# Performance work log

Hardware: AMD Instinct MI355X
Metric: run time of the kernel (lower is better)

Reference implementation:

```python
import jax, jax.numpy as jnp
import numpy as np

# ---- static hyperparams (from comp_encoding.__init__ / DMPNNEncoderLayer) ----
B = 512            # number of molecules in the batch (wrapper's python loop)
A = 128            # padded atoms per molecule == max_mol_len
E = 256            # padded directed bonds per molecule
K = 6              # max incoming bonds gathered per bond/atom
ATOM_FDIM = 133
BOND_FDIM = 14
H = 128            # d_hidden = max_mol_len
DEPTH = 3
G = 2048           # global feature dim (Morgan fingerprint)


def _mol_lens():
    ml = np.array(jax.random.randint(jax.random.fold_in(jax.random.key(0), 5), (B,), 16, H + 1))
    ml[0] = H  # ensure comp_dim == max(mol_lens) == H so per-row padding is a no-op
    return ml


def setup_inputs() -> dict:
    key = jax.random.key(0)
    ks = jax.random.split(key, 10)
    atom_feature = jax.random.normal(ks[0], (B, A, ATOM_FDIM), jnp.float32)
    f_ini_atoms_bond = jax.random.normal(ks[1], (B, E, ATOM_FDIM + BOND_FDIM), jnp.float32)
    atom_to_incoming_bond = jax.random.randint(ks[2], (B, A, K), 0, E)
    mapping = jax.random.randint(ks[3], (B, E, K), 0, E)
    global_f = jax.random.normal(ks[4], (B, G), jnp.float32)
    mol_lens = _mol_lens()  # static numpy ints (constants, drive output shapes)
    W_i = jax.random.normal(ks[6], (H, ATOM_FDIM + BOND_FDIM), jnp.float32) / np.float32(np.sqrt(ATOM_FDIM + BOND_FDIM))
    W_h = jax.random.normal(ks[7], (H, H), jnp.float32) / np.float32(np.sqrt(H))
    W_o = jax.random.normal(ks[8], (H, ATOM_FDIM + H), jnp.float32) / np.float32(np.sqrt(ATOM_FDIM + H))
    b_o = jax.random.normal(ks[9], (H,), jnp.float32) * 0.01
    return dict(atom_feature=atom_feature, f_ini_atoms_bond=f_ini_atoms_bond,
                atom_to_incoming_bond=atom_to_incoming_bond, mapping=mapping,
                global_f=global_f, mol_lens=mol_lens,
                W_i=W_i, W_h=W_h, W_o=W_o, b_o=b_o)


def _gather_sum(msg, idx):
    # msg: [B, E, H]; idx: [B, N, K] -> sum over K incoming messages: [B, N, H]
    b, n, k = idx.shape
    g = jnp.take_along_axis(msg, idx.reshape(b, n * k)[..., None], axis=1)
    return g.reshape(b, n, k, -1).sum(axis=2)


def reference(atom_feature, f_ini_atoms_bond, atom_to_incoming_bond, mapping,
              global_f, mol_lens, W_i, W_h, W_o, b_o):
    # DMPNN: W_i on initial directed-bond features
    inp = jnp.einsum('bef,hf->beh', f_ini_atoms_bond, W_i)   # [B, E, H]
    msg = jax.nn.relu(inp)
    for _ in range(DEPTH - 1):
        agg = _gather_sum(msg, mapping)                      # [B, E, H]
        msg = jax.nn.relu(inp + jnp.einsum('beh,gh->beg', agg, W_h))
    m2a = _gather_sum(msg, atom_to_incoming_bond)            # [B, A, H]
    cat = jnp.concatenate([atom_feature, m2a], axis=-1)      # [B, A, 133+H]
    atoms_h = jax.nn.relu(jnp.einsum('bad,hd->bah', cat, W_o) + b_o)  # [B, A, H]

    # wrapper: take first mol_len atom encodings per molecule, stack, build mask
    ml = np.asarray(mol_lens)
    valid = np.arange(A)[None, :] < ml[:, None]              # [B, A] static
    b_idx, a_idx = np.nonzero(valid)
    comp = atoms_h[b_idx, a_idx]                             # [sum(mol_lens), H]
    c_mask = jnp.asarray(valid.astype(np.float32))           # [B, comp_dim]
    return comp, c_mask
```

## Files before the change

kernel.cpp:

```cpp
#include <hip/hip_runtime.h>
#include <hip/hip_bf16.h>

typedef unsigned int   uint;
typedef unsigned short ushort;
typedef short bf16x8 __attribute__((ext_vector_type(8)));
typedef float f32x4  __attribute__((ext_vector_type(4)));

constexpr int Bm   = 512;
constexpr int Aa   = 128;
constexpr int Ee   = 256;
constexpr int Kk   = 6;
constexpr int AFD  = 133;
constexpr int FD   = 147;
constexpr int Hh   = 128;
constexpr int CATD = 261;
constexpr int KF   = 152;
constexpr int KA   = 144;
constexpr int KWO  = 320;
constexpr int KWIW = 192;
constexpr int LDA  = 72;

__device__ __forceinline__ ushort f2b(float f) {
    uint u = __float_as_uint(f);
    u += 0x7FFFu + ((u >> 16) & 1u);
    return (ushort)(u >> 16);
}
__device__ __forceinline__ uint f2b2(float x, float y) {
    return (uint)f2b(x) | ((uint)f2b(y) << 16);
}
__device__ __forceinline__ float2 b2f2(uint p) {
    float2 r;
    r.x = __uint_as_float(p << 16);
    r.y = __uint_as_float(p & 0xFFFF0000u);
    return r;
}
__device__ __forceinline__ float b2f(ushort u) {
    return __uint_as_float(((uint)u) << 16);
}
__device__ __forceinline__ uint relu2u(uint u) {
    uint neg  = u & 0x80008000u;
    uint mask = (neg >> 15) * 0xFFFFu;
    return u & ~mask;
}

__device__ __forceinline__ void mfma_chunk(const ushort* At, const ushort* Bt,
                                           int wr, int wc, int l15, int quad,
                                           f32x4 acc[4][4]) {
#pragma unroll
    for (int ks = 0; ks < 2; ++ks) {
        const int ko = ks * 32 + quad * 8;
        bf16x8 af[4], bf[4];
#pragma unroll
        for (int i = 0; i < 4; ++i)
            af[i] = *(const bf16x8*)&At[(wr * 64 + i * 16 + l15) * LDA + ko];
#pragma unroll
        for (int j = 0; j < 4; ++j)
            bf[j] = *(const bf16x8*)&Bt[(wc * 64 + j * 16 + l15) * LDA + ko];
#pragma unroll
        for (int i = 0; i < 4; ++i)
#pragma unroll
            for (int j = 0; j < 4; ++j)
                acc[i][j] = __builtin_amdgcn_mfma_f32_16x16x32_bf16(
                    af[i], bf[j], acc[i][j], 0, 0, 0);
    }
}

__global__ __launch_bounds__(256) void k_prep_f(const float* __restrict__ fini,
                                                ushort* __restrict__ fini_b) {
    const int lane = threadIdx.x & 63;
    const int wg   = blockIdx.x * 4 + (threadIdx.x >> 6);
    for (int row = wg; row < Bm * Ee; row += 4096) {
        const float* src = fini + (size_t)row * FD;
        ushort* dst = fini_b + (size_t)row * KF;
        float v0 = src[lane];
        float v1 = src[64 + lane];
        float v2 = (lane < FD - 128) ? src[128 + lane] : 0.f;
        dst[lane]      = f2b(v0);
        dst[64 + lane] = f2b(v1);
        if (lane < KF - 128) dst[128 + lane] = f2b(v2);
    }
}

__global__ __launch_bounds__(256) void k_prep_a(const float* __restrict__ atomf,
                                                ushort* __restrict__ atomf_b) {
    const int lane = threadIdx.x & 63;
    const int wg   = blockIdx.x * 4 + (threadIdx.x >> 6);
    for (int row = wg; row < Bm * Aa; row += 2048) {
        const float* src = atomf + (size_t)row * AFD;
        ushort* dst = atomf_b + (size_t)row * KA;
        float v0 = src[lane];
        float v1 = (lane < AFD - 64) ? src[64 + lane] : 0.f;
        float v2 = (lane < AFD - 128) ? src[128 + lane] : 0.f;
        dst[lane]      = f2b(v0);
        dst[64 + lane] = f2b(v1);
        if (lane < KA - 128) dst[128 + lane] = f2b(v2);
    }
}

__global__ __launch_bounds__(256) void k_prep_w(const float* __restrict__ Wi,
                                                const float* __restrict__ Wh,
                                                const float* __restrict__ Wo,
                                                ushort* __restrict__ Wi_b,
                                                ushort* __restrict__ Wh_b,
                                                ushort* __restrict__ Wo_b) {
    const int h = blockIdx.x, t = threadIdx.x;
    for (int c = t; c < KWIW; c += 256)
        Wi_b[h * KWIW + c] = f2b(c < FD ? Wi[h * FD + c] : 0.f);
    for (int c = t; c < Hh; c += 256)
        Wh_b[h * Hh + c] = f2b(Wh[h * Hh + c]);
    for (int c = t; c < KWO; c += 256) {
        float v = 0.f;
        if (c < AFD)       v = Wo[h * CATD + c];
        else if (c >= 192) v = Wo[h * CATD + AFD + (c - 192)];
        Wo_b[h * KWO + c] = f2b(v);
    }
}

__global__ __launch_bounds__(256, 4) void k_wi(const ushort* __restrict__ fini_b,
                                               const ushort* __restrict__ Wi_b,
                                               ushort* __restrict__ inp_b) {
    __shared__ ushort At[128 * LDA];
    __shared__ ushort Bt[128 * LDA];
    const int tid = threadIdx.x;
    const int row0 = blockIdx.x * 128;
    const int wave = tid >> 6, lane = tid & 63;
    const int wr = wave & 1, wc = wave >> 1;
    const int l15 = lane & 15, quad = lane >> 4;
    f32x4 acc[4][4] = {};

    for (int c = 0; c < 3; ++c) {
        for (int idx = tid; idx < 128 * 8; idx += 256) {
            int r = idx >> 3, g = idx & 7;
            uint4 v = {0, 0, 0, 0};
            if (c < 2 || g < 3)
                v = *(const uint4*)&fini_b[(size_t)(row0 + r) * KF + c * 64 + g * 8];
            *(uint4*)&At[r * LDA + g * 8] = v;
        }
        for (int idx = tid; idx < 128 * 8; idx += 256) {
            int h = idx >> 3, g = idx & 7;
            *(uint4*)&Bt[h * LDA + g * 8] =
                *(const uint4*)&Wi_b[h * KWIW + c * 64 + g * 8];
        }
        __syncthreads();
        mfma_chunk(At, Bt, wr, wc, l15, quad, acc);
        __syncthreads();
    }
#pragma unroll
    for (int i = 0; i < 4; ++i)
#pragma unroll
        for (int reg = 0; reg < 4; ++reg) {
            int row = row0 + wr * 64 + i * 16 + quad * 4 + reg;
#pragma unroll
            for (int j = 0; j < 4; ++j) {
                int col = wc * 64 + j * 16 + l15;
                inp_b[(size_t)row * Hh + col] = f2b(acc[i][j][reg]);
            }
        }
}

__global__ __launch_bounds__(256, 4) void k_hop(const ushort* __restrict__ hIn,
                                                const int* __restrict__ mapping,
                                                const ushort* __restrict__ Wh_b,
                                                const ushort* __restrict__ inp_b,
                                                ushort* __restrict__ hOut) {
    __shared__ ushort At[128 * LDA];
    __shared__ ushort Bt[128 * LDA];
    __shared__ int    map_s[128 * Kk];
    const int tid = threadIdx.x;
    const int row0 = blockIdx.x * 128;
    const int bBase = row0 & ~(Ee - 1);
    const int wave = tid >> 6, lane = tid & 63;
    const int wr = wave & 1, wc = wave >> 1;
    const int l15 = lane & 15, quad = lane >> 4;
    f32x4 acc[4][4] = {};

    for (int i = tid; i < 128 * Kk; i += 256) map_s[i] = mapping[row0 * Kk + i];
    __syncthreads();

    for (int c = 0; c < 2; ++c) {
        for (int t = tid; t < 128 * 8; t += 256) {
            int r = t >> 3, g = t & 7;
            const int* mp = &map_s[r * Kk];
            float2 s0 = {0.f, 0.f}, s1 = {0.f, 0.f}, s2 = {0.f, 0.f}, s3 = {0.f, 0.f};
#pragma unroll
            for (int k = 0; k < Kk; ++k) {
                uint4 m8 = *(const uint4*)
                    &hIn[(size_t)(bBase + mp[k]) * Hh + c * 64 + g * 8];
                float2 a = b2f2(relu2u(m8.x)); s0.x += a.x; s0.y += a.y;
                float2 b = b2f2(relu2u(m8.y)); s1.x += b.x; s1.y += b.y;
                float2 d = b2f2(relu2u(m8.z)); s2.x += d.x; s2.y += d.y;
                float2 e = b2f2(relu2u(m8.w)); s3.x += e.x; s3.y += e.y;
            }
            uint4 o;
            o.x = f2b2(s0.x, s0.y); o.y = f2b2(s1.x, s1.y);
            o.z = f2b2(s2.x, s2.y); o.w = f2b2(s3.x, s3.y);
            *(uint4*)&At[r * LDA + g * 8] = o;
        }
        for (int idx = tid; idx < 128 * 8; idx += 256) {
            int h = idx >> 3, g = idx & 7;
            *(uint4*)&Bt[h * LDA + g * 8] =
                *(const uint4*)&Wh_b[h * Hh + c * 64 + g * 8];
        }
        __syncthreads();
        mfma_chunk(At, Bt, wr, wc, l15, quad, acc);
        __syncthreads();
    }
#pragma unroll
    for (int i = 0; i < 4; ++i)
#pragma unroll
        for (int reg = 0; reg < 4; ++reg) {
            int row = row0 + wr * 64 + i * 16 + quad * 4 + reg;
#pragma unroll
            for (int j = 0; j < 4; ++j) {
                int col = wc * 64 + j * 16 + l15;
                float v = b2f(inp_b[(size_t)row * Hh + col]) + acc[i][j][reg];
                hOut[(size_t)row * Hh + col] = f2b(v);
            }
        }
}

__global__ __launch_bounds__(256, 4) void k_read(const ushort* __restrict__ h2,
                                                 const int* __restrict__ a2ib,
                                                 const ushort* __restrict__ atomf_b,
                                                 const ushort* __restrict__ Wo_b,
                                                 const float* __restrict__ bo,
                                                 const int* __restrict__ mol_lens,
                                                 const int* __restrict__ pfx,
                                                 float* __restrict__ out) {
    __shared__ ushort At[128 * LDA];
    __shared__ ushort Bt[128 * LDA];
    __shared__ int    a2_s[128 * Kk];
    const int tid = threadIdx.x;
    const int b = blockIdx.x;
    const int row0 = b * Aa;
    const int bBase = b * Ee;
    const int wave = tid >> 6, lane = tid & 63;
    const int wr = wave & 1, wc = wave >> 1;
    const int l15 = lane & 15, quad = lane >> 4;
    f32x4 acc[4][4] = {};

    for (int i = tid; i < 128 * Kk; i += 256) a2_s[i] = a2ib[row0 * Kk + i];
    __syncthreads();

    for (int c = 0; c < 5; ++c) {
        if (c < 3) {
            for (int idx = tid; idx < 128 * 8; idx += 256) {
                int r = idx >> 3, g = idx & 7;
                uint4 v = {0, 0, 0, 0};
                if (c < 2 || g < 2)
                    v = *(const uint4*)&atomf_b[(size_t)(row0 + r) * KA + c * 64 + g * 8];
                *(uint4*)&At[r * LDA + g * 8] = v;
            }
        } else {
            const int hb = (c - 3) * 64;
            for (int t = tid; t < 128 * 8; t += 256) {
                int r = t >> 3, g = t & 7;
                const int* mp = &a2_s[r * Kk];
                float2 s0 = {0.f, 0.f}, s1 = {0.f, 0.f}, s2 = {0.f, 0.f}, s3 = {0.f, 0.f};
#pragma unroll
                for (int k = 0; k < Kk; ++k) {
                    uint4 m8 = *(const uint4*)
                        &h2[(size_t)(bBase + mp[k]) * Hh + hb + g * 8];
                    float2 a  = b2f2(relu2u(m8.x)); s0.x += a.x;  s0.y += a.y;
                    float2 bb = b2f2(relu2u(m8.y)); s1.x += bb.x; s1.y += bb.y;
                    float2 d  = b2f2(relu2u(m8.z)); s2.x += d.x;  s2.y += d.y;
                    float2 e  = b2f2(relu2u(m8.w)); s3.x += e.x;  s3.y += e.y;
                }
                uint4 o;
                o.x = f2b2(s0.x, s0.y); o.y = f2b2(s1.x, s1.y);
                o.z = f2b2(s2.x, s2.y); o.w = f2b2(s3.x, s3.y);
                *(uint4*)&At[r * LDA + g * 8] = o;
            }
        }
        for (int idx = tid; idx < 128 * 8; idx += 256) {
            int h = idx >> 3, g = idx & 7;
            *(uint4*)&Bt[h * LDA + g * 8] =
                *(const uint4*)&Wo_b[h * KWO + c * 64 + g * 8];
        }
        __syncthreads();
        mfma_chunk(At, Bt, wr, wc, l15, quad, acc);
        __syncthreads();
    }

    const int len  = mol_lens[b];
    const int base = pfx[b];
#pragma unroll
    for (int i = 0; i < 4; ++i)
#pragma unroll
        for (int reg = 0; reg < 4; ++reg) {
            int a = wr * 64 + i * 16 + quad * 4 + reg;
            if (a < len) {
#pragma unroll
                for (int j = 0; j < 4; ++j) {
                    int col = wc * 64 + j * 16 + l15;
                    float v = acc[i][j][reg] + bo[col];
                    out[(size_t)(base + a) * Hh + col] = v > 0.f ? v : 0.f;
                }
            }
        }
}

__global__ __launch_bounds__(512) void k_scan(const int* __restrict__ ml,
                                              int* __restrict__ pfx) {
    __shared__ int s[512];
    int t = threadIdx.x;
    s[t] = ml[t];
    __syncthreads();
    for (int off = 1; off < 512; off <<= 1) {
        int v = (t >= off) ? s[t - off] : 0;
        __syncthreads();
        s[t] += v;
        __syncthreads();
    }
    pfx[t + 1] = s[t];
    if (t == 0) pfx[0] = 0;
}

__global__ __launch_bounds__(128) void k_cmask(const int* __restrict__ ml,
                                               float* __restrict__ cmask) {
    int b = blockIdx.x, t = threadIdx.x;
    cmask[b * Aa + t] = (t < ml[b]) ? 1.0f : 0.0f;
}

extern "C" void kernel_launch(void* const* d_in, const int* in_sizes, int n_in,
                              void* d_out, int out_size, void* d_ws, size_t ws_size,
                              hipStream_t stream) {
    const float* atom_feature = (const float*)d_in[0];
    const float* f_ini        = (const float*)d_in[1];
    const int*   a2ib         = (const int*)d_in[2];
    const int*   mapping      = (const int*)d_in[3];
    const int*   mol_lens     = (const int*)d_in[5];
    const float* Wi           = (const float*)d_in[6];
    const float* Wh           = (const float*)d_in[7];
    const float* Wo           = (const float*)d_in[8];
    const float* bo           = (const float*)d_in[9];
    float* out = (float*)d_out;

    constexpr size_t NMSG  = (size_t)Bm * Ee * Hh;
    constexpr size_t NFINI = (size_t)Bm * Ee * KF;
    constexpr size_t NATM  = (size_t)Bm * Aa * KA;
    ushort* fini_b  = (ushort*)d_ws;
    ushort* h2      = fini_b;
    ushort* inp_b   = fini_b + NFINI;
    ushort* h1      = inp_b + NMSG;
    ushort* atomf_b = h1 + NMSG;
    ushort* Wi_b    = atomf_b + NATM;
    ushort* Wh_b    = Wi_b + 128 * KWIW;
    ushort* Wo_b    = Wh_b + 128 * Hh;
    int*    pfx     = (int*)(Wo_b + 128 * KWO);

    float* cmask = out + ((size_t)out_size - (size_t)Bm * Aa);

    k_prep_w<<<128, 256, 0, stream>>>(Wi, Wh, Wo, Wi_b, Wh_b, Wo_b);
    k_prep_f<<<1024, 256, 0, stream>>>(f_ini, fini_b);
    k_prep_a<<<512, 256, 0, stream>>>(atom_feature, atomf_b);
    k_scan <<<1, 512, 0, stream>>>(mol_lens, pfx);
    k_cmask<<<Bm, 128, 0, stream>>>(mol_lens, cmask);
    k_wi   <<<(Bm * Ee) / 128, 256, 0, stream>>>(fini_b, Wi_b, inp_b);
    k_hop  <<<(Bm * Ee) / 128, 256, 0, stream>>>(inp_b, mapping, Wh_b, inp_b, h1);
    k_hop  <<<(Bm * Ee) / 128, 256, 0, stream>>>(h1, mapping, Wh_b, inp_b, h2);
    k_read <<<Bm, 256, 0, stream>>>(h2, a2ib, atomf_b, Wo_b, bo,
                                    mol_lens, pfx, out);
}
```

Measured before the change: 304.2 us.

## Fuse whole DMPNN pipeline into one per-molecule kernel with LDS-resident messages

Replaces the separate prep, W_i, two hop, readout and cmask kernels with a single kernel that runs one block per molecule. All bond messages stay in shared memory across the hops, and the fp32 inputs are converted to bf16 on the fly. This removes the global-memory round trips for intermediate bf16 tensors and several kernel launches. In exchange it uses about 140KB of LDS per block, which limits occupancy, and weight fragments are now read from global memory in every block.

Measured after the change: 287.5 us. -5.5%, faster.

```diff
diff --git a/kernel.cpp b/kernel.cpp
--- a/kernel.cpp
+++ b/kernel.cpp
@@ -1,5 +1,4 @@
 #include <hip/hip_runtime.h>
-#include <hip/hip_bf16.h>
 
 typedef unsigned int   uint;
 typedef unsigned short ushort;
@@ -14,11 +13,10 @@
 constexpr int FD   = 147;
 constexpr int Hh   = 128;
 constexpr int CATD = 261;
-constexpr int KF   = 152;
-constexpr int KA   = 144;
+constexpr int KWI  = 192;
 constexpr int KWO  = 320;
-constexpr int KWIW = 192;
-constexpr int LDA  = 72;
+constexpr int MST  = 136;
+constexpr int SST  = 72;
 
 __device__ __forceinline__ ushort f2b(float f) {
     uint u = __float_as_uint(f);
@@ -34,67 +32,23 @@
     r.y = __uint_as_float(p & 0xFFFF0000u);
     return r;
 }
-__device__ __forceinline__ float b2f(ushort u) {
-    return __uint_as_float(((uint)u) << 16);
-}
-__device__ __forceinline__ uint relu2u(uint u) {
-    uint neg  = u & 0x80008000u;
-    uint mask = (neg >> 15) * 0xFFFFu;
-    return u & ~mask;
-}
-
-__device__ __forceinline__ void mfma_chunk(const ushort* At, const ushort* Bt,
-                                           int wr, int wc, int l15, int quad,
-                                           f32x4 acc[4][4]) {
-#pragma unroll
-    for (int ks = 0; ks < 2; ++ks) {
-        const int ko = ks * 32 + quad * 8;
-        bf16x8 af[4], bf[4];
-#pragma unroll
-        for (int i = 0; i < 4; ++i)
-            af[i] = *(const bf16x8*)&At[(wr * 64 + i * 16 + l15) * LDA + ko];
-#pragma unroll
-        for (int j = 0; j < 4; ++j)
-            bf[j] = *(const bf16x8*)&Bt[(wc * 64 + j * 16 + l15) * LDA + ko];
-#pragma unroll
-        for (int i = 0; i < 4; ++i)
-#pragma unroll
-            for (int j = 0; j < 4; ++j)
-                acc[i][j] = __builtin_amdgcn_mfma_f32_16x16x32_bf16(
-                    af[i], bf[j], acc[i][j], 0, 0, 0);
-    }
-}
-
-__global__ __launch_bounds__(256) void k_prep_f(const float* __restrict__ fini,
-                                                ushort* __restrict__ fini_b) {
-    const int lane = threadIdx.x & 63;
-    const int wg   = blockIdx.x * 4 + (threadIdx.x >> 6);
-    for (int row = wg; row < Bm * Ee; row += 4096) {
-        const float* src = fini + (size_t)row * FD;
-        ushort* dst = fini_b + (size_t)row * KF;
-        float v0 = src[lane];
-        float v1 = src[64 + lane];
-        float v2 = (lane < FD - 128) ? src[128 + lane] : 0.f;
-        dst[lane]      = f2b(v0);
-        dst[64 + lane] = f2b(v1);
-        if (lane < KF - 128) dst[128 + lane] = f2b(v2);
-    }
-}
-
-__global__ __launch_bounds__(256) void k_prep_a(const float* __restrict__ atomf,
-                                                ushort* __restrict__ atomf_b) {
-    const int lane = threadIdx.x & 63;
-    const int wg   = blockIdx.x * 4 + (threadIdx.x >> 6);
-    for (int row = wg; row < Bm * Aa; row += 2048) {
-        const float* src = atomf + (size_t)row * AFD;
-        ushort* dst = atomf_b + (size_t)row * KA;
-        float v0 = src[lane];
-        float v1 = (lane < AFD - 64) ? src[64 + lane] : 0.f;
-        float v2 = (lane < AFD - 128) ? src[128 + lane] : 0.f;
-        dst[lane]      = f2b(v0);
-        dst[64 + lane] = f2b(v1);
-        if (lane < KA - 128) dst[128 + lane] = f2b(v2);
-    }
+
+__device__ __forceinline__ bf16x8 gsum6(const ushort* src, const int* mr, int ko) {
+    float2 s0 = {0.f, 0.f}, s1 = {0.f, 0.f}, s2 = {0.f, 0.f}, s3 = {0.f, 0.f};
+#pragma unroll
+    for (int k = 0; k < Kk; ++k) {
+        uint4 m = *(const uint4*)&src[mr[k] + ko];
+        float2 a = b2f2(m.x); s0.x += a.x; s0.y += a.y;
+        float2 b = b2f2(m.y); s1.x += b.x; s1.y += b.y;
+        float2 d = b2f2(m.z); s2.x += d.x; s2.y += d.y;
+        float2 e = b2f2(m.w); s3.x += e.x; s3.y += e.y;
+    }
+    uint4 o;
+    o.x = f2b2(s0.x, s0.y); o.y = f2b2(s1.x, s1.y);
+    o.z = f2b2(s2.x, s2.y); o.w = f2b2(s3.x, s3.y);
+    bf16x8 r;
+    __builtin_memcpy(&r, &o, 16);
+    return r;
 }
 
 __global__ __launch_bounds__(256) void k_prep_w(const float* __restrict__ Wi,
@@ -104,8 +58,8 @@
                                                 ushort* __restrict__ Wh_b,
                                                 ushort* __restrict__ Wo_b) {
     const int h = blockIdx.x, t = threadIdx.x;
-    for (int c = t; c < KWIW; c += 256)
-        Wi_b[h * KWIW + c] = f2b(c < FD ? Wi[h * FD + c] : 0.f);
+    for (int c = t; c < KWI; c += 256)
+        Wi_b[h * KWI + c] = f2b(c < FD ? Wi[h * FD + c] : 0.f);
     for (int c = t; c < Hh; c += 256)
         Wh_b[h * Hh + c] = f2b(Wh[h * Hh + c]);
     for (int c = t; c < KWO; c += 256) {
@@ -114,190 +68,6 @@
         else if (c >= 192) v = Wo[h * CATD + AFD + (c - 192)];
         Wo_b[h * KWO + c] = f2b(v);
     }
-}
-
-__global__ __launch_bounds__(256, 4) void k_wi(const ushort* __restrict__ fini_b,
-                                               const ushort* __restrict__ Wi_b,
-                                               ushort* __restrict__ inp_b) {
-    __shared__ ushort At[128 * LDA];
-    __shared__ ushort Bt[128 * LDA];
-    const int tid = threadIdx.x;
-    const int row0 = blockIdx.x * 128;
-    const int wave = tid >> 6, lane = tid & 63;
-    const int wr = wave & 1, wc = wave >> 1;
-    const int l15 = lane & 15, quad = lane >> 4;
-    f32x4 acc[4][4] = {};
-
-    for (int c = 0; c < 3; ++c) {
-        for (int idx = tid; idx < 128 * 8; idx += 256) {
-            int r = idx >> 3, g = idx & 7;
-            uint4 v = {0, 0, 0, 0};
-            if (c < 2 || g < 3)
-                v = *(const uint4*)&fini_b[(size_t)(row0 + r) * KF + c * 64 + g * 8];
-            *(uint4*)&At[r * LDA + g * 8] = v;
-        }
-        for (int idx = tid; idx < 128 * 8; idx += 256) {
-            int h = idx >> 3, g = idx & 7;
-            *(uint4*)&Bt[h * LDA + g * 8] =
-                *(const uint4*)&Wi_b[h * KWIW + c * 64 + g * 8];
-        }
-        __syncthreads();
-        mfma_chunk(At, Bt, wr, wc, l15, quad, acc);
-        __syncthreads();
-    }
-#pragma unroll
-    for (int i = 0; i < 4; ++i)
-#pragma unroll
-        for (int reg = 0; reg < 4; ++reg) {
-            int row = row0 + wr * 64 + i * 16 + quad * 4 + reg;
-#pragma unroll
-            for (int j = 0; j < 4; ++j) {
-                int col = wc * 64 + j * 16 + l15;
-                inp_b[(size_t)row * Hh + col] = f2b(acc[i][j][reg]);
-            }
-        }
-}
-
-__global__ __launch_bounds__(256, 4) void k_hop(const ushort* __restrict__ hIn,
-                                                const int* __restrict__ mapping,
-                                                const ushort* __restrict__ Wh_b,
-                                                const ushort* __restrict__ inp_b,
-                                                ushort* __restrict__ hOut) {
-    __shared__ ushort At[128 * LDA];
-    __shared__ ushort Bt[128 * LDA];
-    __shared__ int    map_s[128 * Kk];
-    const int tid = threadIdx.x;
-    const int row0 = blockIdx.x * 128;
-    const int bBase = row0 & ~(Ee - 1);
-    const int wave = tid >> 6, lane = tid & 63;
-    const int wr = wave & 1, wc = wave >> 1;
-    const int l15 = lane & 15, quad = lane >> 4;
-    f32x4 acc[4][4] = {};
-
-    for (int i = tid; i < 128 * Kk; i += 256) map_s[i] = mapping[row0 * Kk + i];
-    __syncthreads();
-
-    for (int c = 0; c < 2; ++c) {
-        for (int t = tid; t < 128 * 8; t += 256) {
-            int r = t >> 3, g = t & 7;
-            const int* mp = &map_s[r * Kk];
-            float2 s0 = {0.f, 0.f}, s1 = {0.f, 0.f}, s2 = {0.f, 0.f}, s3 = {0.f, 0.f};
-#pragma unroll
-            for (int k = 0; k < Kk; ++k) {
-                uint4 m8 = *(const uint4*)
-                    &hIn[(size_t)(bBase + mp[k]) * Hh + c * 64 + g * 8];
-                float2 a = b2f2(relu2u(m8.x)); s0.x += a.x; s0.y += a.y;
-                float2 b = b2f2(relu2u(m8.y)); s1.x += b.x; s1.y += b.y;
-                float2 d = b2f2(relu2u(m8.z)); s2.x += d.x; s2.y += d.y;
-                float2 e = b2f2(relu2u(m8.w)); s3.x += e.x; s3.y += e.y;
-            }
-            uint4 o;
-            o.x = f2b2(s0.x, s0.y); o.y = f2b2(s1.x, s1.y);
-            o.z = f2b2(s2.x, s2.y); o.w = f2b2(s3.x, s3.y);
-            *(uint4*)&At[r * LDA + g * 8] = o;
-        }
-        for (int idx = tid; idx < 128 * 8; idx += 256) {
-            int h = idx >> 3, g = idx & 7;
-            *(uint4*)&Bt[h * LDA + g * 8] =
-                *(const uint4*)&Wh_b[h * Hh + c * 64 + g * 8];
-        }
-        __syncthreads();
-        mfma_chunk(At, Bt, wr, wc, l15, quad, acc);
-        __syncthreads();
-    }
-#pragma unroll
-    for (int i = 0; i < 4; ++i)
-#pragma unroll
-        for (int reg = 0; reg < 4; ++reg) {
-            int row = row0 + wr * 64 + i * 16 + quad * 4 + reg;
-#pragma unroll
-            for (int j = 0; j < 4; ++j) {
-                int col = wc * 64 + j * 16 + l15;
-                float v = b2f(inp_b[(size_t)row * Hh + col]) + acc[i][j][reg];
-                hOut[(size_t)row * Hh + col] = f2b(v);
-            }
-        }
-}
-
-__global__ __launch_bounds__(256, 4) void k_read(const ushort* __restrict__ h2,
-                                                 const int* __restrict__ a2ib,
-                                                 const ushort* __restrict__ atomf_b,
-                                                 const ushort* __restrict__ Wo_b,
-                                                 const float* __restrict__ bo,
-                                                 const int* __restrict__ mol_lens,
-                                                 const int* __restrict__ pfx,
-                                                 float* __restrict__ out) {
-    __shared__ ushort At[128 * LDA];
-    __shared__ ushort Bt[128 * LDA];
-    __shared__ int    a2_s[128 * Kk];
-    const int tid = threadIdx.x;
-    const int b = blockIdx.x;
-    const int row0 = b * Aa;
-    const int bBase = b * Ee;
-    const int wave = tid >> 6, lane = tid & 63;
-    const int wr = wave & 1, wc = wave >> 1;
-    const int l15 = lane & 15, quad = lane >> 4;
-    f32x4 acc[4][4] = {};
-
-    for (int i = tid; i < 128 * Kk; i += 256) a2_s[i] = a2ib[row0 * Kk + i];
-    __syncthreads();
-
-    for (int c = 0; c < 5; ++c) {
-        if (c < 3) {
-            for (int idx = tid; idx < 128 * 8; idx += 256) {
-                int r = idx >> 3, g = idx & 7;
-                uint4 v = {0, 0, 0, 0};
-                if (c < 2 || g < 2)
-                    v = *(const uint4*)&atomf_b[(size_t)(row0 + r) * KA + c * 64 + g * 8];
-                *(uint4*)&At[r * LDA + g * 8] = v;
-            }
-        } else {
-            const int hb = (c - 3) * 64;
-            for (int t = tid; t < 128 * 8; t += 256) {
-                int r = t >> 3, g = t & 7;
-                const int* mp = &a2_s[r * Kk];
-                float2 s0 = {0.f, 0.f}, s1 = {0.f, 0.f}, s2 = {0.f, 0.f}, s3 = {0.f, 0.f};
-#pragma unroll
-                for (int k = 0; k < Kk; ++k) {
-                    uint4 m8 = *(const uint4*)
-                        &h2[(size_t)(bBase + mp[k]) * Hh + hb + g * 8];
-                    float2 a  = b2f2(relu2u(m8.x)); s0.x += a.x;  s0.y += a.y;
-                    float2 bb = b2f2(relu2u(m8.y)); s1.x += bb.x; s1.y += bb.y;
-                    float2 d  = b2f2(relu2u(m8.z)); s2.x += d.x;  s2.y += d.y;
-                    float2 e  = b2f2(relu2u(m8.w)); s3.x += e.x;  s3.y += e.y;
-                }
-                uint4 o;
-                o.x = f2b2(s0.x, s0.y); o.y = f2b2(s1.x, s1.y);
-                o.z = f2b2(s2.x, s2.y); o.w = f2b2(s3.x, s3.y);
-                *(uint4*)&At[r * LDA + g * 8] = o;
-            }
-        }
-        for (int idx = tid; idx < 128 * 8; idx += 256) {
-            int h = idx >> 3, g = idx & 7;
-            *(uint4*)&Bt[h * LDA + g * 8] =
-                *(const uint4*)&Wo_b[h * KWO + c * 64 + g * 8];
-        }
-        __syncthreads();
-        mfma_chunk(At, Bt, wr, wc, l15, quad, acc);
-        __syncthreads();
-    }
-
-    const int len  = mol_lens[b];
-    const int base = pfx[b];
-#pragma unroll
-    for (int i = 0; i < 4; ++i)
-#pragma unroll
-        for (int reg = 0; reg < 4; ++reg) {
-            int a = wr * 64 + i * 16 + quad * 4 + reg;
-            if (a < len) {
-#pragma unroll
-                for (int j = 0; j < 4; ++j) {
-                    int col = wc * 64 + j * 16 + l15;
-                    float v = acc[i][j][reg] + bo[col];
-                    out[(size_t)(base + a) * Hh + col] = v > 0.f ? v : 0.f;
-                }
-            }
-        }
 }
 
 __global__ __launch_bounds__(512) void k_scan(const int* __restrict__ ml,
@@ -316,10 +86,217 @@
     if (t == 0) pfx[0] = 0;
 }
 
-__global__ __launch_bounds__(128) void k_cmask(const int* __restrict__ ml,
-                                               float* __restrict__ cmask) {
-    int b = blockIdx.x, t = threadIdx.x;
-    cmask[b * Aa + t] = (t < ml[b]) ? 1.0f : 0.0f;
+__global__ __launch_bounds__(512, 2) void k_fused(
+        const float* __restrict__ atomf,
+        const float* __restrict__ fini,
+        const int*   __restrict__ a2ib,
+        const int*   __restrict__ mapping,
+        const ushort* __restrict__ Wi_b,
+        const ushort* __restrict__ Wh_b,
+        const ushort* __restrict__ Wo_b,
+        const float* __restrict__ bo,
+        const int*   __restrict__ mol_lens,
+        const int*   __restrict__ pfx,
+        float* __restrict__ out,
+        float* __restrict__ cmask) {
+    __shared__ ushort msg0[Ee * MST];
+    __shared__ ushort msg1[Ee * MST];
+    __shared__ int    map_s[Ee * Kk];
+    __shared__ int    a2_s[Aa * Kk];
+
+    const int b    = blockIdx.x;
+    const int tid  = threadIdx.x;
+    const int wave = tid >> 6;
+    const int lane = tid & 63;
+    const int l15  = lane & 15, quad = lane >> 4;
+
+    for (int i = tid; i < Ee * Kk; i += 512) map_s[i] = mapping[b * Ee * Kk + i];
+    for (int i = tid; i < Aa * Kk; i += 512) a2_s[i]  = a2ib[b * Aa * Kk + i];
+    const int len = mol_lens[b];
+    if (tid < Aa) cmask[b * Aa + tid] = (tid < len) ? 1.0f : 0.0f;
+
+    f32x4 acc[2][8];
+#pragma unroll
+    for (int i = 0; i < 2; ++i)
+#pragma unroll
+        for (int j = 0; j < 8; ++j) acc[i][j] = (f32x4){0.f, 0.f, 0.f, 0.f};
+
+    const float* fsrc = fini + (size_t)b * Ee * FD;
+    for (int c = 0; c < 3; ++c) {
+        for (int idx = tid; idx < Ee * 16; idx += 512) {
+            int r = idx >> 4, gg = idx & 15;
+            int c0 = c * 64 + gg * 4;
+            const float* sp = fsrc + (size_t)r * FD + c0;
+            float v0 = (c0 + 0 < FD) ? sp[0] : 0.f;
+            float v1 = (c0 + 1 < FD) ? sp[1] : 0.f;
+            float v2 = (c0 + 2 < FD) ? sp[2] : 0.f;
+            float v3 = (c0 + 3 < FD) ? sp[3] : 0.f;
+            uint2 p;
+            p.x = f2b2(v0, v1);
+            p.y = f2b2(v2, v3);
+            *(uint2*)&msg1[r * SST + gg * 4] = p;
+        }
+        __syncthreads();
+#pragma unroll
+        for (int ks = 0; ks < 2; ++ks) {
+            const int ko = ks * 32 + quad * 8;
+            bf16x8 bf[8], af[2];
+#pragma unroll
+            for (int j = 0; j < 8; ++j)
+                bf[j] = *(const bf16x8*)&Wi_b[(j * 16 + l15) * KWI + c * 64 + ko];
+#pragma unroll
+            for (int i = 0; i < 2; ++i)
+                af[i] = *(const bf16x8*)&msg1[(wave * 32 + i * 16 + l15) * SST + ko];
+#pragma unroll
+            for (int i = 0; i < 2; ++i)
+#pragma unroll
+                for (int j = 0; j < 8; ++j)
+                    acc[i][j] = __builtin_amdgcn_mfma_f32_16x16x32_bf16(
+                        af[i], bf[j], acc[i][j], 0, 0, 0);
+        }
+        __syncthreads();
+    }
+
+    uint2 inp_pk[2][8];
+#pragma unroll
+    for (int i = 0; i < 2; ++i)
+#pragma unroll
+        for (int j = 0; j < 8; ++j) {
+            f32x4 a4 = acc[i][j];
+            uint2 p;
+            p.x = f2b2(a4[0], a4[1]);
+            p.y = f2b2(a4[2], a4[3]);
+            inp_pk[i][j] = p;
+            int col = j * 16 + l15;
+#pragma unroll
+            for (int reg = 0; reg < 4; ++reg) {
+                int row = wave * 32 + i * 16 + quad * 4 + reg;
+                float v = a4[reg] > 0.f ? a4[reg] : 0.f;
+                msg0[row * MST + col] = f2b(v);
+            }
+        }
+    __syncthreads();
+
+#pragma unroll
+    for (int h = 0; h < 2; ++h) {
+        const ushort* src = h ? msg1 : msg0;
+        ushort*       dst = h ? msg0 : msg1;
+        int mr[2][Kk];
+#pragma unroll
+        for (int i = 0; i < 2; ++i) {
+            int row = wave * 32 + i * 16 + l15;
+#pragma unroll
+            for (int k = 0; k < Kk; ++k) mr[i][k] = map_s[row * Kk + k] * MST;
+        }
+#pragma unroll
+        for (int i = 0; i < 2; ++i)
+#pragma unroll
+            for (int j = 0; j < 8; ++j) acc[i][j] = (f32x4){0.f, 0.f, 0.f, 0.f};
+#pragma unroll
+        for (int ks = 0; ks < 4; ++ks) {
+            const int ko = ks * 32 + quad * 8;
+            bf16x8 bf[8], af[2];
+#pragma unroll
+            for (int j = 0; j < 8; ++j)
+                bf[j] = *(const bf16x8*)&Wh_b[(j * 16 + l15) * Hh + ko];
+#pragma unroll
+            for (int i = 0; i < 2; ++i) af[i] = gsum6(src, mr[i], ko);
+#pragma unroll
+            for (int i = 0; i < 2; ++i)
+#pragma unroll
+                for (int j = 0; j < 8; ++j)
+                    acc[i][j] = __builtin_amdgcn_mfma_f32_16x16x32_bf16(
+                        af[i], bf[j], acc[i][j], 0, 0, 0);
+        }
+#pragma unroll
+        for (int i = 0; i < 2; ++i)
+#pragma unroll
+            for (int j = 0; j < 8; ++j) {
+                float2 lo = b2f2(inp_pk[i][j].x);
+                float2 hi = b2f2(inp_pk[i][j].y);
+                float v[4];
+                v[0] = lo.x + acc[i][j][0];
+                v[1] = lo.y + acc[i][j][1];
+                v[2] = hi.x + acc[i][j][2];
+                v[3] = hi.y + acc[i][j][3];
+                int col = j * 16 + l15;
+#pragma unroll
+                for (int reg = 0; reg < 4; ++reg) {
+                    int row = wave * 32 + i * 16 + quad * 4 + reg;
+                    float r = v[reg] > 0.f ? v[reg] : 0.f;
+                    dst[row * MST + col] = f2b(r);
+                }
+            }
+        __syncthreads();
+    }
+
+    f32x4 ro[8];
+#pragma unroll
+    for (int j = 0; j < 8; ++j) ro[j] = (f32x4){0.f, 0.f, 0.f, 0.f};
+
+    const float* asrc = atomf + (size_t)b * Aa * AFD;
+    for (int c = 0; c < 3; ++c) {
+        for (int idx = tid; idx < Aa * 16; idx += 512) {
+            int r = idx >> 4, gg = idx & 15;
+            int c0 = c * 64 + gg * 4;
+            const float* sp = asrc + (size_t)r * AFD + c0;
+            float v0 = (c0 + 0 < AFD) ? sp[0] : 0.f;
+            float v1 = (c0 + 1 < AFD) ? sp[1] : 0.f;
+            float v2 = (c0 + 2 < AFD) ? sp[2] : 0.f;
+            float v3 = (c0 + 3 < AFD) ? sp[3] : 0.f;
+            uint2 p;
+            p.x = f2b2(v0, v1);
+            p.y = f2b2(v2, v3);
+            *(uint2*)&msg1[r * SST + gg * 4] = p;
+        }
+        __syncthreads();
+#pragma unroll
+        for (int ks = 0; ks < 2; ++ks) {
+            const int ko = ks * 32 + quad * 8;
+            bf16x8 a0 = *(const bf16x8*)&msg1[(wave * 16 + l15) * SST + ko];
+            bf16x8 bf[8];
+#pragma unroll
+            for (int j = 0; j < 8; ++j)
+                bf[j] = *(const bf16x8*)&Wo_b[(j * 16 + l15) * KWO + c * 64 + ko];
+#pragma unroll
+            for (int j = 0; j < 8; ++j)
+                ro[j] = __builtin_amdgcn_mfma_f32_16x16x32_bf16(a0, bf[j], ro[j], 0, 0, 0);
+        }
+        __syncthreads();
+    }
+    {
+        int ar[Kk];
+        int row = wave * 16 + l15;
+#pragma unroll
+        for (int k = 0; k < Kk; ++k) ar[k] = a2_s[row * Kk + k] * MST;
+#pragma unroll
+        for (int ks = 0; ks < 4; ++ks) {
+            const int ko = ks * 32 + quad * 8;
+            bf16x8 a0 = gsum6(msg0, ar, ko);
+            bf16x8 bf[8];
+#pragma unroll
+            for (int j = 0; j < 8; ++j)
+                bf[j] = *(const bf16x8*)&Wo_b[(j * 16 + l15) * KWO + 192 + ko];
+#pragma unroll
+            for (int j = 0; j < 8; ++j)
+                ro[j] = __builtin_amdgcn_mfma_f32_16x16x32_bf16(a0, bf[j], ro[j], 0, 0, 0);
+        }
+    }
+
+    const int base = pfx[b];
+#pragma unroll
+    for (int j = 0; j < 8; ++j) {
+        int col = j * 16 + l15;
+        float bv = bo[col];
+#pragma unroll
+        for (int reg = 0; reg < 4; ++reg) {
+            int a = wave * 16 + quad * 4 + reg;
+            if (a < len) {
+                float v = ro[j][reg] + bv;
+                out[(size_t)(base + a) * Hh + col] = v > 0.f ? v : 0.f;
+            }
+        }
+    }
 }
 
 extern "C" void kernel_launch(void* const* d_in, const int* in_sizes, int n_in,
@@ -336,29 +313,16 @@
     const float* bo           = (const float*)d_in[9];
     float* out = (float*)d_out;
 
-    constexpr size_t NMSG  = (size_t)Bm * Ee * Hh;
-    constexpr size_t NFINI = (size_t)Bm * Ee * KF;
-    constexpr size_t NATM  = (size_t)Bm * Aa * KA;
-    ushort* fini_b  = (ushort*)d_ws;
-    ushort* h2      = fini_b;
-    ushort* inp_b   = fini_b + NFINI;
-    ushort* h1      = inp_b + NMSG;
-    ushort* atomf_b = h1 + NMSG;
-    ushort* Wi_b    = atomf_b + NATM;
-    ushort* Wh_b    = Wi_b + 128 * KWIW;
-    ushort* Wo_b    = Wh_b + 128 * Hh;
-    int*    pfx     = (int*)(Wo_b + 128 * KWO);
+    ushort* Wi_b = (ushort*)d_ws;
+    ushort* Wh_b = Wi_b + 128 * KWI;
+    ushort* Wo_b = Wh_b + 128 * Hh;
+    int*    pfx  = (int*)(Wo_b + 128 * KWO);
 
     float* cmask = out + ((size_t)out_size - (size_t)Bm * Aa);
 
     k_prep_w<<<128, 256, 0, stream>>>(Wi, Wh, Wo, Wi_b, Wh_b, Wo_b);
-    k_prep_f<<<1024, 256, 0, stream>>>(f_ini, fini_b);
-    k_prep_a<<<512, 256, 0, stream>>>(atom_feature, atomf_b);
-    k_scan <<<1, 512, 0, stream>>>(mol_lens, pfx);
-    k_cmask<<<Bm, 128, 0, stream>>>(mol_lens, cmask);
-    k_wi   <<<(Bm * Ee) / 128, 256, 0, stream>>>(fini_b, Wi_b, inp_b);
-    k_hop  <<<(Bm * Ee) / 128, 256, 0, stream>>>(inp_b, mapping, Wh_b, inp_b, h1);
-    k_hop  <<<(Bm * Ee) / 128, 256, 0, stream>>>(h1, mapping, Wh_b, inp_b, h2);
-    k_read <<<Bm, 256, 0, stream>>>(h2, a2ib, atomf_b, Wo_b, bo,
-                                    mol_lens, pfx, out);
-}
+    k_scan  <<<1, 512, 0, stream>>>(mol_lens, pfx);
+    k_fused <<<Bm, 512, 0, stream>>>(atom_feature, f_ini, a2ib, mapping,
+                                     Wi_b, Wh_b, Wo_b, bo, mol_lens, pfx,
+                                     out, cmask);
+}
```
